# Kernel tuning notes

Hardware: AMD Instinct MI355X
Metric: run time of the kernel (lower is better)

The kernel has to match this reference:

```python
import jax, jax.numpy as jnp
from jax import lax
import numpy as np


def _edt_to(zero_mask):
    """Exact Euclidean distance from every pixel to the nearest True pixel of
    zero_mask. Equivalent to scipy.ndimage.distance_transform_edt(~zero_mask).
    Separable two-pass algorithm: 1-D distance along W (two scans), then an
    exact lower-envelope min along H using squared distances.
    zero_mask: bool [B, H, W] -> float32 [B, H, W].
    """
    B, H, W = zero_mask.shape
    INF = jnp.float32(H + W)  # larger than any attainable 1-D distance
    bg = jnp.transpose(zero_mask, (2, 0, 1))  # [W, B, H]: scan over W

    def step(c, b):
        c = jnp.where(b, 0.0, c + 1.0)
        return c, c

    init = jnp.full((B, H), INF, dtype=jnp.float32)
    _, f = lax.scan(step, init, bg)                 # left-to-right
    _, r = lax.scan(step, init, bg, reverse=True)   # right-to-left
    d1 = jnp.minimum(f, r)                          # [W, B, H] 1-D dist along W
    g = jnp.transpose(d1 * d1, (1, 2, 0))           # [B, H, W] squared 1-D dist

    # d2[b, y, x] = min_{y'} g[b, y', x] + (y - y')^2   (exact 2-D squared EDT)
    yy = jnp.arange(H, dtype=jnp.float32)
    dy2 = (yy[:, None] - yy[None, :]) ** 2          # [H, H']
    d2 = jnp.min(g[:, None, :, :] + dy2[None, :, :, None], axis=2)  # [B, H, W]
    return jnp.sqrt(d2)


def _boundary_loss(preds, targets, idx_class=None):
    B, C, H, W = preds.shape
    probs = jax.nn.softmax(preds, axis=1)
    classes = [idx_class] if idx_class is not None else list(range(1, C))
    total = jnp.float32(0.0)
    count = jnp.float32(0.0)
    for cls in classes:
        pos = targets == cls        # bool [B, H, W]
        neg = ~pos
        has = jnp.any(pos)
        # scipy: distance(negmask)*negmask - (distance(posmask)-1)*posmask
        # distance_transform_edt(negmask) == dist to nearest pos pixel, etc.
        dmap = _edt_to(pos) * neg - (_edt_to(neg) - 1.0) * pos
        loss = jnp.mean(dmap * probs[:, cls])
        total = total + jnp.where(has, loss, 0.0)
        count = count + has.astype(jnp.float32)
    return jnp.where(count > 0, total / jnp.maximum(count, 1.0), jnp.float32(0.0))


def setup_inputs() -> dict:
    key = jax.random.key(0)
    k1, k2 = jax.random.split(key)
    preds = jax.random.normal(k1, (8, 4, 256, 256), dtype=jnp.float32)
    targets = jax.random.randint(k2, (8, 256, 256), 0, 4)
    return {"preds": preds, "targets": targets}


def reference(preds, targets):
    return _boundary_loss(preds, targets, idx_class=None)
```

## Files before the change

### kernel.cpp

```cpp
#include <hip/hip_runtime.h>
#include <math.h>

#define BB 8
#define HH 256
#define WW 256
#define T  2
#define NW 4
#define PAD 96
#define LDSW (WW + 2 * PAD)

typedef unsigned long long u64;

__global__ __launch_bounds__(256) void build_masks(const int* __restrict__ tgt,
                                                   u64* __restrict__ masks,
                                                   float* __restrict__ out) {
  const int x = threadIdx.x;
  const int b = blockIdx.x;
  const int w = blockIdx.y;
  if (b == 0 && w == 0 && x == 0) out[0] = 0.0f;
  u64 m0 = 0, m1 = 0, m2 = 0, m3 = 0, bit = 1ull;
  const int* p = tgt + ((size_t)b * HH + w * 64) * WW + x;
  for (int ly = 0; ly < 64; ++ly, bit += bit) {
    int e = p[ly * WW];
    m0 |= (e == 0) ? bit : 0ull;
    m1 |= (e == 1) ? bit : 0ull;
    m2 |= (e == 2) ? bit : 0ull;
    m3 |= (e == 3) ? bit : 0ull;
  }
  u64* mp = masks + ((size_t)(b * NW + w) * WW + x) * 4;
  ulonglong2 lo, hi;
  lo.x = m0; lo.y = m1;
  hi.x = m2; hi.y = m3;
  *(ulonglong2*)(mp + 0) = lo;
  *(ulonglong2*)(mp + 2) = hi;
}

__global__ __launch_bounds__(256, 4) void fused(const u64* __restrict__ masks,
                                                const int* __restrict__ tgt,
                                                const float* __restrict__ preds,
                                                float* __restrict__ out) {
  __shared__ float g[T][LDSW][4];
  __shared__ float fred[4];
  const int x  = threadIdx.x;
  const int b  = blockIdx.x;
  const int y0 = blockIdx.y * T;
  const int wy = y0 >> 6;

  for (int i = x; i < T * 2 * PAD; i += 256) {
    int j = i / (2 * PAD);
    int q = i - j * (2 * PAD);
    int idx = (q < PAD) ? q : (q + WW);
    *(float4*)&g[j][idx][0] = make_float4(1e30f, 1e30f, 1e30f, 1e30f);
  }

  u64 m[NW][4];
  {
    const u64* mb = masks + ((size_t)b * NW * WW + x) * 4;
#pragma unroll
    for (int w = 0; w < NW; ++w) {
      ulonglong2 lo = *(const ulonglong2*)(mb + (size_t)w * WW * 4 + 0);
      ulonglong2 hi = *(const ulonglong2*)(mb + (size_t)w * WW * 4 + 2);
      m[w][0] = lo.x; m[w][1] = lo.y; m[w][2] = hi.x; m[w][3] = hi.y;
    }
  }

  float d[T][4];
  int lmax = 0;
#pragma unroll
  for (int j = 0; j < T; ++j) {
    const int y  = y0 + j;
    const int ly = y & 63;
    const int ini = min(513 + y, 768 - y);
    float4 gv;
    float* gp = (float*)&gv;
#pragma unroll
    for (int k = 0; k < 4; ++k) {
      int best = ini;
#pragma unroll
      for (int w = 0; w < NW; ++w) {
        u64 bits = m[w][k];
        if (w < wy) {
          int dd = y - (w * 64 + 63 - __clzll((long long)bits));
          best = min(best, bits ? dd : 1024);
        } else if (w > wy) {
          int dd = w * 64 + (__ffsll((long long)bits) - 1) - y;
          best = min(best, bits ? dd : 1024);
        } else {
          u64 lo = bits & ((2ull << ly) - 1ull);
          u64 hi = bits >> ly;
          int dl = ly - 63 + __clzll((long long)lo);
          int dh = __ffsll((long long)hi) - 1;
          best = min(best, lo ? dl : 1024);
          best = min(best, hi ? dh : 1024);
        }
      }
      lmax = max(lmax, best);
      gp[k] = (float)(best * best);
      d[j][k] = gp[k];
    }
    *(float4*)&g[j][x + PAD][0] = gv;
  }

#pragma unroll
  for (int off = 32; off; off >>= 1) lmax = max(lmax, __shfl_xor(lmax, off, 64));
  const int R  = __builtin_amdgcn_readfirstlane(lmax);
  const int Rw = min(R, PAD);
  __syncthreads();

  float pr[T][4];
  int   tt[T];
#pragma unroll
  for (int j = 0; j < T; ++j) {
    const int y = y0 + j;
    tt[j] = tgt[((size_t)b * HH + y) * WW + x];
    const float* pb = preds + ((size_t)b * 4 * HH + y) * WW + x;
    pr[j][0] = pb[0 * HH * WW];
    pr[j][1] = pb[1 * HH * WW];
    pr[j][2] = pb[2 * HH * WW];
    pr[j][3] = pb[3 * HH * WW];
  }

  for (int kk = 1; kk <= Rw; ++kk) {
    float fkk = (float)kk;
    float fk2 = fkk * fkk;
#pragma unroll
    for (int j = 0; j < T; ++j) {
      float4 gm = *(const float4*)&g[j][x + PAD - kk][0];
      float4 gp = *(const float4*)&g[j][x + PAD + kk][0];
      d[j][0] = fminf(d[j][0], fminf(gm.x, gp.x) + fk2);
      d[j][1] = fminf(d[j][1], fminf(gm.y, gp.y) + fk2);
      d[j][2] = fminf(d[j][2], fminf(gm.z, gp.z) + fk2);
      d[j][3] = fminf(d[j][3], fminf(gm.w, gp.w) + fk2);
    }
  }
  if (R > PAD) {
#pragma unroll 1
    for (int kk = PAD + 1; kk <= R; ++kk) {
      int xm = max(x - kk, 0), xp = min(x + kk, WW - 1);
      float dm = (float)(x - xm), dpq = (float)(xp - x);
      float dm2 = dm * dm, dp2 = dpq * dpq;
#pragma unroll
      for (int j = 0; j < T; ++j) {
        float4 gm = *(const float4*)&g[j][xm + PAD][0];
        float4 gp = *(const float4*)&g[j][xp + PAD][0];
        d[j][0] = fminf(d[j][0], fminf(gm.x + dm2, gp.x + dp2));
        d[j][1] = fminf(d[j][1], fminf(gm.y + dm2, gp.y + dp2));
        d[j][2] = fminf(d[j][2], fminf(gm.z + dm2, gp.z + dp2));
        d[j][3] = fminf(d[j][3], fminf(gm.w + dm2, gp.w + dp2));
      }
    }
  }

  float acc = 0.0f;
#pragma unroll
  for (int j = 0; j < T; ++j) {
    const int t = tt[j];
    float p0 = pr[j][0], p1 = pr[j][1], p2 = pr[j][2], p3 = pr[j][3];
    float pm = fmaxf(fmaxf(p0, p1), fmaxf(p2, p3));
    float e0 = expf(p0 - pm), e1 = expf(p1 - pm);
    float e2 = expf(p2 - pm), e3 = expf(p3 - pm);
    float inv = 1.0f / (e0 + e1 + e2 + e3);

    float dn1 = fminf(d[j][0], fminf(d[j][2], d[j][3]));
    float dn2 = fminf(d[j][0], fminf(d[j][1], d[j][3]));
    float dn3 = fminf(d[j][0], fminf(d[j][1], d[j][2]));
    float c1 = (t == 1) ? (1.0f - sqrtf(dn1)) : sqrtf(d[j][1]);
    float c2 = (t == 2) ? (1.0f - sqrtf(dn2)) : sqrtf(d[j][2]);
    float c3 = (t == 3) ? (1.0f - sqrtf(dn3)) : sqrtf(d[j][3]);
    acc += (c1 * e1 + c2 * e2 + c3 * e3) * inv;
  }

#pragma unroll
  for (int off = 32; off; off >>= 1) acc += __shfl_down(acc, off, 64);
  if ((x & 63) == 0) fred[x >> 6] = acc;
  __syncthreads();
  if (x == 0)
    atomicAdd(out, (fred[0] + fred[1] + fred[2] + fred[3]) *
                       (1.0f / (3.0f * BB * HH * WW)));
}

extern "C" void kernel_launch(void* const* d_in, const int* in_sizes, int n_in,
                              void* d_out, int out_size, void* d_ws, size_t ws_size,
                              hipStream_t stream) {
  const float* preds = (const float*)d_in[0];
  const int*   tgt   = (const int*)d_in[1];
  float* out   = (float*)d_out;
  u64*   masks = (u64*)d_ws;

  build_masks<<<dim3(BB, NW), 256, 0, stream>>>(tgt, masks, out);
  fused<<<dim3(BB, HH / T), 256, 0, stream>>>(masks, tgt, preds, out);
}
```

Measured before the change: 85.65 us.

## Add early-exit horizontal scan, split mask build, derive targets from bitmasks

The horizontal min-plus loop now ends early once every lane's running minima are no larger than the current squared offset, since no further column can improve them. The mask-building kernel is split across two half-tiles of 32 rows so more blocks run in parallel. The fused kernel no longer re-reads targets and instead recovers the class from the packed bitmasks. The preds loads are issued earlier to overlap with the mask decode. The extra per-iteration max reduction and wave vote add a little ALU work in exchange for skipping iterations.

```diff
diff --git a/kernel.cpp b/kernel.cpp
--- a/kernel.cpp
+++ b/kernel.cpp
@@ -12,31 +12,30 @@
 typedef unsigned long long u64;
 
 __global__ __launch_bounds__(256) void build_masks(const int* __restrict__ tgt,
-                                                   u64* __restrict__ masks,
+                                                   unsigned* __restrict__ masks32,
                                                    float* __restrict__ out) {
   const int x = threadIdx.x;
   const int b = blockIdx.x;
   const int w = blockIdx.y;
-  if (b == 0 && w == 0 && x == 0) out[0] = 0.0f;
-  u64 m0 = 0, m1 = 0, m2 = 0, m3 = 0, bit = 1ull;
-  const int* p = tgt + ((size_t)b * HH + w * 64) * WW + x;
-  for (int ly = 0; ly < 64; ++ly, bit += bit) {
-    int e = p[ly * WW];
-    m0 |= (e == 0) ? bit : 0ull;
-    m1 |= (e == 1) ? bit : 0ull;
-    m2 |= (e == 2) ? bit : 0ull;
-    m3 |= (e == 3) ? bit : 0ull;
+  const int h = blockIdx.z;
+  if (b == 0 && w == 0 && h == 0 && x == 0) out[0] = 0.0f;
+  unsigned m0 = 0, m1 = 0, m2 = 0, m3 = 0, bit = 1u;
+  const int* p = tgt + ((size_t)b * HH + w * 64 + h * 32) * WW + x;
+  for (int r = 0; r < 32; ++r, bit += bit) {
+    int e = p[r * WW];
+    m0 |= (e == 0) ? bit : 0u;
+    m1 |= (e == 1) ? bit : 0u;
+    m2 |= (e == 2) ? bit : 0u;
+    m3 |= (e == 3) ? bit : 0u;
   }
-  u64* mp = masks + ((size_t)(b * NW + w) * WW + x) * 4;
-  ulonglong2 lo, hi;
-  lo.x = m0; lo.y = m1;
-  hi.x = m2; hi.y = m3;
-  *(ulonglong2*)(mp + 0) = lo;
-  *(ulonglong2*)(mp + 2) = hi;
+  unsigned* mp = masks32 + (((size_t)(b * NW + w) * WW + x) * 4) * 2 + h;
+  mp[0] = m0;
+  mp[2] = m1;
+  mp[4] = m2;
+  mp[6] = m3;
 }
 
 __global__ __launch_bounds__(256, 4) void fused(const u64* __restrict__ masks,
-                                                const int* __restrict__ tgt,
                                                 const float* __restrict__ preds,
                                                 float* __restrict__ out) {
   __shared__ float g[T][LDSW][4];
@@ -45,13 +44,6 @@
   const int b  = blockIdx.x;
   const int y0 = blockIdx.y * T;
   const int wy = y0 >> 6;
-
-  for (int i = x; i < T * 2 * PAD; i += 256) {
-    int j = i / (2 * PAD);
-    int q = i - j * (2 * PAD);
-    int idx = (q < PAD) ? q : (q + WW);
-    *(float4*)&g[j][idx][0] = make_float4(1e30f, 1e30f, 1e30f, 1e30f);
-  }
 
   u64 m[NW][4];
   {
@@ -62,6 +54,23 @@
       ulonglong2 hi = *(const ulonglong2*)(mb + (size_t)w * WW * 4 + 2);
       m[w][0] = lo.x; m[w][1] = lo.y; m[w][2] = hi.x; m[w][3] = hi.y;
     }
+  }
+
+  float pr[T][4];
+#pragma unroll
+  for (int j = 0; j < T; ++j) {
+    const float* pb = preds + ((size_t)b * 4 * HH + (y0 + j)) * WW + x;
+    pr[j][0] = pb[0 * HH * WW];
+    pr[j][1] = pb[1 * HH * WW];
+    pr[j][2] = pb[2 * HH * WW];
+    pr[j][3] = pb[3 * HH * WW];
+  }
+
+  for (int i = x; i < T * 2 * PAD; i += 256) {
+    int j = i / (2 * PAD);
+    int q = i - j * (2 * PAD);
+    int idx = (q < PAD) ? q : (q + WW);
+    *(float4*)&g[j][idx][0] = make_float4(1e30f, 1e30f, 1e30f, 1e30f);
   }
 
   float d[T][4];
@@ -107,22 +116,11 @@
   const int Rw = min(R, PAD);
   __syncthreads();
 
-  float pr[T][4];
-  int   tt[T];
-#pragma unroll
-  for (int j = 0; j < T; ++j) {
-    const int y = y0 + j;
-    tt[j] = tgt[((size_t)b * HH + y) * WW + x];
-    const float* pb = preds + ((size_t)b * 4 * HH + y) * WW + x;
-    pr[j][0] = pb[0 * HH * WW];
-    pr[j][1] = pb[1 * HH * WW];
-    pr[j][2] = pb[2 * HH * WW];
-    pr[j][3] = pb[3 * HH * WW];
-  }
-
+  bool alldone = false;
   for (int kk = 1; kk <= Rw; ++kk) {
     float fkk = (float)kk;
     float fk2 = fkk * fkk;
+    float dmax = 0.0f;
 #pragma unroll
     for (int j = 0; j < T; ++j) {
       float4 gm = *(const float4*)&g[j][x + PAD - kk][0];
@@ -131,14 +129,17 @@
       d[j][1] = fminf(d[j][1], fminf(gm.y, gp.y) + fk2);
       d[j][2] = fminf(d[j][2], fminf(gm.z, gp.z) + fk2);
       d[j][3] = fminf(d[j][3], fminf(gm.w, gp.w) + fk2);
+      dmax = fmaxf(dmax, fmaxf(fmaxf(d[j][0], d[j][1]), fmaxf(d[j][2], d[j][3])));
     }
+    if (__all(dmax <= fk2)) { alldone = true; break; }
   }
-  if (R > PAD) {
+  if (!alldone && R > PAD) {
 #pragma unroll 1
     for (int kk = PAD + 1; kk <= R; ++kk) {
       int xm = max(x - kk, 0), xp = min(x + kk, WW - 1);
       float dm = (float)(x - xm), dpq = (float)(xp - x);
       float dm2 = dm * dm, dp2 = dpq * dpq;
+      float dmax = 0.0f;
 #pragma unroll
       for (int j = 0; j < T; ++j) {
         float4 gm = *(const float4*)&g[j][xm + PAD][0];
@@ -147,14 +148,20 @@
         d[j][1] = fminf(d[j][1], fminf(gm.y + dm2, gp.y + dp2));
         d[j][2] = fminf(d[j][2], fminf(gm.z + dm2, gp.z + dp2));
         d[j][3] = fminf(d[j][3], fminf(gm.w + dm2, gp.w + dp2));
+        dmax = fmaxf(dmax, fmaxf(fmaxf(d[j][0], d[j][1]), fmaxf(d[j][2], d[j][3])));
       }
+      float fkk = (float)kk;
+      if (__all(dmax <= fkk * fkk)) break;
     }
   }
 
   float acc = 0.0f;
 #pragma unroll
   for (int j = 0; j < T; ++j) {
-    const int t = tt[j];
+    const int ly = (y0 + j) & 63;
+    const int t = (int)((m[wy][1] >> ly) & 1ull) * 1 +
+                  (int)((m[wy][2] >> ly) & 1ull) * 2 +
+                  (int)((m[wy][3] >> ly) & 1ull) * 3;
     float p0 = pr[j][0], p1 = pr[j][1], p2 = pr[j][2], p3 = pr[j][3];
     float pm = fmaxf(fmaxf(p0, p1), fmaxf(p2, p3));
     float e0 = expf(p0 - pm), e1 = expf(p1 - pm);
@@ -187,6 +194,6 @@
   float* out   = (float*)d_out;
   u64*   masks = (u64*)d_ws;
 
-  build_masks<<<dim3(BB, NW), 256, 0, stream>>>(tgt, masks, out);
-  fused<<<dim3(BB, HH / T), 256, 0, stream>>>(masks, tgt, preds, out);
+  build_masks<<<dim3(BB, NW, 2), 256, 0, stream>>>(tgt, (unsigned*)masks, out);
+  fused<<<dim3(BB, HH / T), 256, 0, stream>>>(masks, preds, out);
 }
```

New measurement: 80.59 us. 1.06x faster.
